# Kernel tuning notes

Hardware: AMD Instinct MI355X
Metric: run time of the kernel (lower is better)

Reference implementation:

```python
import jax, jax.numpy as jnp
import numpy as np

NEG_INF = -10000.0  # matches the original max_val init
EPS = 1e-8          # torch.nn.CosineSimilarity default eps


def setup_inputs() -> dict:
    key = jax.random.key(0)
    k1, k2, k3 = jax.random.split(key, 3)
    B, S, H = 32, 1024, 1024
    seq = jax.random.normal(k1, (B, S, H), dtype=jnp.float32)
    # sep0 = index of first [SEP] (end of question), sep1 = end of passage
    sep0 = jax.random.randint(k2, (B, 1), 32, 128)
    sep1 = jax.random.randint(k3, (B, 1), 768, S)
    idxs = jnp.concatenate([sep0, sep1], axis=1).astype(jnp.int64)
    return {"sequence_outputs": seq, "idxs": idxs, "max_ans_len": 32}


def reference(sequence_outputs, idxs, max_ans_len):
    # sequence_outputs: [B, S, H] float; idxs: [B, 2] int (sep0, sep1)
    B, S, H = sequence_outputs.shape
    L = max_ans_len
    sep0 = idxs[:, 0]
    sep1 = idxs[:, 1]

    # question_cat_repr = cat(seq[1], seq[sep0-1]); cos over the 2H concat
    # decomposes as (h_i.q1 + h_j.q2) / (sqrt(|h_i|^2+|h_j|^2) * |q|)
    q1 = sequence_outputs[:, 1, :]                                   # [B, H]
    q2 = jnp.take_along_axis(
        sequence_outputs, (sep0 - 1)[:, None, None], axis=1)[:, 0, :]  # [B, H]
    qn2 = jnp.sum(q1 * q1, -1) + jnp.sum(q2 * q2, -1)                # [B]

    d1 = jnp.einsum('bsh,bh->bs', sequence_outputs, q1)             # [B, S]
    d2 = jnp.einsum('bsh,bh->bs', sequence_outputs, q2)             # [B, S]
    n2 = jnp.sum(sequence_outputs * sequence_outputs, -1)           # [B, S]

    # banded window: for start i, ends j = i + l, l in [0, L)
    i = jnp.arange(S)[:, None]                                      # [S, 1]
    l = jnp.arange(L)[None, :]                                      # [1, L]
    j = jnp.minimum(i + l, S - 1)                                   # [S, L]
    d2w = d2[:, j]                                                  # [B, S, L]
    n2w = n2[:, j]                                                  # [B, S, L]

    denom = jnp.maximum(
        jnp.sqrt((n2[:, :, None] + n2w) * qn2[:, None, None]), EPS)
    sim = (d1[:, :, None] + d2w) / denom                            # [B, S, L]

    # valid ends: j = i + l < min(sep1, i + L); (i+l >= S implies invalid too)
    valid_j = (i + l)[None, :, :] < sep1[:, None, None]
    sim = jnp.where(valid_j, sim, NEG_INF)

    max_vals = jnp.max(sim, axis=-1)                                # [B, S]
    end_idx = jnp.arange(S)[None, :] + jnp.argmax(sim, axis=-1)     # [B, S]

    # valid starts: sep0 + 1 <= i < sep1
    pos = jnp.arange(S)[None, :]
    valid_i = (pos > sep0[:, None]) & (pos < sep1[:, None])
    max_vals = jnp.where(valid_i, max_vals, NEG_INF)
    end_idx = jnp.where(valid_i, end_idx, -1)
    return max_vals, end_idx
```

## Files before the change

kernel.cpp:

```cpp
#include <hip/hip_runtime.h>

#define NEG_INF_F (-10000.0f)
#define EPS_F (1e-8f)

typedef float f4 __attribute__((ext_vector_type(4)));

template <int H>
__global__ __launch_bounds__(256) void row_stats_pipe(
    const float* __restrict__ seq, const int* __restrict__ idxs,
    float* __restrict__ d1, float* __restrict__ d2, float* __restrict__ n2,
    int S, int nrows) {
  constexpr int NF4 = H / 4;
  constexpr int C = H / 256;
  constexpr int R = 4;
  int wave = blockIdx.x * 4 + (threadIdx.x >> 6);
  int lane = threadIdx.x & 63;
  int row0 = wave * R;
  if (row0 >= nrows) return;

  int b = row0 / S;
  int sep0 = idxs[2 * b];

  const f4* base = reinterpret_cast<const f4*>(seq);
  const f4* q1p = base + ((size_t)b * S + 1) * NF4 + lane;
  const f4* q2p = base + ((size_t)b * S + (sep0 - 1)) * NF4 + lane;
  const f4* rp = base + (size_t)row0 * NF4 + lane;

  f4 q1f[C], q2f[C], x[2][C];
  #pragma unroll
  for (int i = 0; i < C; ++i) q1f[i] = q1p[i * 64];
  #pragma unroll
  for (int i = 0; i < C; ++i) q2f[i] = q2p[i * 64];
  #pragma unroll
  for (int i = 0; i < C; ++i) x[0][i] = __builtin_nontemporal_load(rp + i * 64);

  #pragma unroll
  for (int r = 0; r < R; ++r) {
    if (r + 1 < R) {
      const f4* np = rp + (size_t)(r + 1) * NF4;
      #pragma unroll
      for (int i = 0; i < C; ++i)
        x[(r + 1) & 1][i] = __builtin_nontemporal_load(np + i * 64);
    }
    float s1 = 0.f, s2 = 0.f, sn = 0.f;
    #pragma unroll
    for (int i = 0; i < C; ++i) {
      f4 v = x[r & 1][i];
      s1 += v[0] * q1f[i][0] + v[1] * q1f[i][1] + v[2] * q1f[i][2] + v[3] * q1f[i][3];
      s2 += v[0] * q2f[i][0] + v[1] * q2f[i][1] + v[2] * q2f[i][2] + v[3] * q2f[i][3];
      sn += v[0] * v[0] + v[1] * v[1] + v[2] * v[2] + v[3] * v[3];
    }
    #pragma unroll
    for (int off = 32; off >= 1; off >>= 1) {
      s1 += __shfl_xor(s1, off, 64);
      s2 += __shfl_xor(s2, off, 64);
      sn += __shfl_xor(sn, off, 64);
    }
    if (lane == 0) {
      d1[row0 + r] = s1;
      d2[row0 + r] = s2;
      n2[row0 + r] = sn;
    }
  }
}

__global__ __launch_bounds__(256) void row_stats_kernel(
    const float* __restrict__ seq, const int* __restrict__ idxs,
    float* __restrict__ d1, float* __restrict__ d2, float* __restrict__ n2,
    int B, int S, int H) {
  int gtid = blockIdx.x * blockDim.x + threadIdx.x;
  int row = gtid >> 6;
  int lane = threadIdx.x & 63;
  int nrows = B * S;
  if (row >= nrows) return;

  int b = row / S;
  int sep0 = idxs[b * 2 + 0];

  const float* rowp = seq + (size_t)row * H;
  const float* q1p = seq + ((size_t)b * S + 1) * H;
  const float* q2p = seq + ((size_t)b * S + (sep0 - 1)) * H;

  float s1 = 0.f, s2 = 0.f, sn = 0.f;
  for (int h = lane * 4; h < H; h += 64 * 4) {
    float4 x = *reinterpret_cast<const float4*>(rowp + h);
    float4 a = *reinterpret_cast<const float4*>(q1p + h);
    float4 c = *reinterpret_cast<const float4*>(q2p + h);
    s1 += x.x * a.x + x.y * a.y + x.z * a.z + x.w * a.w;
    s2 += x.x * c.x + x.y * c.y + x.z * c.z + x.w * c.w;
    sn += x.x * x.x + x.y * x.y + x.z * x.z + x.w * x.w;
  }
  #pragma unroll
  for (int off = 32; off >= 1; off >>= 1) {
    s1 += __shfl_xor(s1, off, 64);
    s2 += __shfl_xor(s2, off, 64);
    sn += __shfl_xor(sn, off, 64);
  }
  if (lane == 0) {
    d1[row] = s1;
    d2[row] = s2;
    n2[row] = sn;
  }
}

template <int L>
__global__ __launch_bounds__(256) void window_max_wave(
    const float* __restrict__ d1, const float* __restrict__ d2,
    const float* __restrict__ n2, const int* __restrict__ idxs,
    float* __restrict__ out, int S, int nrows) {
  int wave = blockIdx.x * 4 + (threadIdx.x >> 6);
  int lane = threadIdx.x & 63;
  int h = lane >> 5;
  int l = lane & 31;
  int t = wave * 2 + h;
  if (t >= nrows) return;
  int b = t / S;
  int s = t - b * S;

  int sep0 = idxs[b * 2 + 0];
  int sep1 = idxs[b * 2 + 1];

  size_t bS = (size_t)b * S;
  float qn2 = n2[bS + 1] + n2[bS + (sep0 - 1)];
  float my_d1 = d1[t];
  float my_n2 = n2[t];

  int j = min(s + l, S - 1);
  float w2 = n2[bS + j];
  float v2 = d2[bS + j];
  float prod = (my_n2 + w2) * qn2;
  float sim = (my_d1 + v2) * __frsqrt_rn(fmaxf(prod, EPS_F * EPS_F));
  sim = (s + l < sep1) ? sim : NEG_INF_F;

  float best = sim;
  int best_l = l;
  #pragma unroll
  for (int off = 16; off >= 1; off >>= 1) {
    float ov = __shfl_xor(best, off, 64);
    int oi = __shfl_xor(best_l, off, 64);
    if (ov > best || (ov == best && oi < best_l)) {
      best = ov;
      best_l = oi;
    }
  }

  if (l == 0) {
    bool valid_i = (s > sep0) && (s < sep1);
    out[t] = valid_i ? best : NEG_INF_F;
    out[nrows + t] = valid_i ? (float)(s + best_l) : -1.0f;
  }
}

extern "C" void kernel_launch(void* const* d_in, const int* in_sizes, int n_in,
                              void* d_out, int out_size, void* d_ws, size_t ws_size,
                              hipStream_t stream) {
  const float* seq = (const float*)d_in[0];
  const int* idxs = (const int*)d_in[1];
  const int* pL = (const int*)d_in[2];

  int B = in_sizes[1] / 2;
  int S = out_size / (2 * B);
  int H = (int)((long long)in_sizes[0] / ((long long)B * S));
  int nrows = B * S;

  float* d1 = (float*)d_ws;
  float* d2 = d1 + nrows;
  float* n2 = d2 + nrows;

  if (H == 1024 && (S % 4) == 0 && (nrows % 16) == 0) {
    int gridA = nrows / 16;
    row_stats_pipe<1024><<<gridA, 256, 0, stream>>>(seq, idxs, d1, d2, n2, S,
                                                    nrows);
  } else {
    int gridA = (nrows + 3) / 4;
    row_stats_kernel<<<gridA, 256, 0, stream>>>(seq, idxs, d1, d2, n2, B, S, H);
  }

  int gridB = (nrows + 7) / 8;
  window_max_wave<32><<<gridB, 256, 0, stream>>>(d1, d2, n2, idxs,
                                                 (float*)d_out, S, nrows);
  (void)pL;
}
```

Measured before the change: 31.99 us.

## Stage query rows in LDS and compute window max one start per thread

```diff
diff --git a/kernel.cpp b/kernel.cpp
--- a/kernel.cpp
+++ b/kernel.cpp
@@ -6,31 +6,30 @@
 typedef float f4 __attribute__((ext_vector_type(4)));
 
 template <int H>
-__global__ __launch_bounds__(256) void row_stats_pipe(
+__global__ __launch_bounds__(256, 8) void row_stats_ldsq(
     const float* __restrict__ seq, const int* __restrict__ idxs,
     float* __restrict__ d1, float* __restrict__ d2, float* __restrict__ n2,
     int S, int nrows) {
   constexpr int NF4 = H / 4;
   constexpr int C = H / 256;
   constexpr int R = 4;
-  int wave = blockIdx.x * 4 + (threadIdx.x >> 6);
-  int lane = threadIdx.x & 63;
+  __shared__ f4 q1s[NF4];
+  __shared__ f4 q2s[NF4];
+
+  int tid = threadIdx.x;
+  int lane = tid & 63;
+  int wave = blockIdx.x * 4 + (tid >> 6);
   int row0 = wave * R;
-  if (row0 >= nrows) return;
-
-  int b = row0 / S;
+  int b = (blockIdx.x * 16) / S;
   int sep0 = idxs[2 * b];
 
   const f4* base = reinterpret_cast<const f4*>(seq);
-  const f4* q1p = base + ((size_t)b * S + 1) * NF4 + lane;
-  const f4* q2p = base + ((size_t)b * S + (sep0 - 1)) * NF4 + lane;
+  q1s[tid] = base[((size_t)b * S + 1) * NF4 + tid];
+  q2s[tid] = base[((size_t)b * S + (sep0 - 1)) * NF4 + tid];
+  __syncthreads();
+
   const f4* rp = base + (size_t)row0 * NF4 + lane;
-
-  f4 q1f[C], q2f[C], x[2][C];
-  #pragma unroll
-  for (int i = 0; i < C; ++i) q1f[i] = q1p[i * 64];
-  #pragma unroll
-  for (int i = 0; i < C; ++i) q2f[i] = q2p[i * 64];
+  f4 x[2][C];
   #pragma unroll
   for (int i = 0; i < C; ++i) x[0][i] = __builtin_nontemporal_load(rp + i * 64);
 
@@ -46,8 +45,10 @@
     #pragma unroll
     for (int i = 0; i < C; ++i) {
       f4 v = x[r & 1][i];
-      s1 += v[0] * q1f[i][0] + v[1] * q1f[i][1] + v[2] * q1f[i][2] + v[3] * q1f[i][3];
-      s2 += v[0] * q2f[i][0] + v[1] * q2f[i][1] + v[2] * q2f[i][2] + v[3] * q2f[i][3];
+      f4 a = q1s[i * 64 + lane];
+      f4 c = q2s[i * 64 + lane];
+      s1 += v[0] * a[0] + v[1] * a[1] + v[2] * a[2] + v[3] * a[3];
+      s2 += v[0] * c[0] + v[1] * c[1] + v[2] * c[2] + v[3] * c[3];
       sn += v[0] * v[0] + v[1] * v[1] + v[2] * v[2] + v[3] * v[3];
     }
     #pragma unroll
@@ -104,15 +105,11 @@
 }
 
 template <int L>
-__global__ __launch_bounds__(256) void window_max_wave(
+__global__ __launch_bounds__(64) void window_max_fast(
     const float* __restrict__ d1, const float* __restrict__ d2,
     const float* __restrict__ n2, const int* __restrict__ idxs,
     float* __restrict__ out, int S, int nrows) {
-  int wave = blockIdx.x * 4 + (threadIdx.x >> 6);
-  int lane = threadIdx.x & 63;
-  int h = lane >> 5;
-  int l = lane & 31;
-  int t = wave * 2 + h;
+  int t = blockIdx.x * 64 + threadIdx.x;
   if (t >= nrows) return;
   int b = t / S;
   int s = t - b * S;
@@ -125,30 +122,25 @@
   float my_d1 = d1[t];
   float my_n2 = n2[t];
 
-  int j = min(s + l, S - 1);
-  float w2 = n2[bS + j];
-  float v2 = d2[bS + j];
-  float prod = (my_n2 + w2) * qn2;
-  float sim = (my_d1 + v2) * __frsqrt_rn(fmaxf(prod, EPS_F * EPS_F));
-  sim = (s + l < sep1) ? sim : NEG_INF_F;
+  const float* d2b = d2 + bS;
+  const float* n2b = n2 + bS;
 
-  float best = sim;
-  int best_l = l;
+  float best = NEG_INF_F;
+  int best_l = 0;
   #pragma unroll
-  for (int off = 16; off >= 1; off >>= 1) {
-    float ov = __shfl_xor(best, off, 64);
-    int oi = __shfl_xor(best_l, off, 64);
-    if (ov > best || (ov == best && oi < best_l)) {
-      best = ov;
-      best_l = oi;
-    }
+  for (int l = 0; l < L; ++l) {
+    int j = min(s + l, S - 1);
+    float w2 = n2b[j];
+    float v2 = d2b[j];
+    float prod = (my_n2 + w2) * qn2;
+    float sim = (my_d1 + v2) * __frsqrt_rn(fmaxf(prod, EPS_F * EPS_F));
+    sim = (s + l < sep1) ? sim : NEG_INF_F;
+    if (sim > best) { best = sim; best_l = l; }
   }
 
-  if (l == 0) {
-    bool valid_i = (s > sep0) && (s < sep1);
-    out[t] = valid_i ? best : NEG_INF_F;
-    out[nrows + t] = valid_i ? (float)(s + best_l) : -1.0f;
-  }
+  bool valid_i = (s > sep0) && (s < sep1);
+  out[t] = valid_i ? best : NEG_INF_F;
+  out[nrows + t] = valid_i ? (float)(s + best_l) : -1.0f;
 }
 
 extern "C" void kernel_launch(void* const* d_in, const int* in_sizes, int n_in,
@@ -167,17 +159,17 @@
   float* d2 = d1 + nrows;
   float* n2 = d2 + nrows;
 
-  if (H == 1024 && (S % 4) == 0 && (nrows % 16) == 0) {
+  if (H == 1024 && (S % 16) == 0 && (nrows % 16) == 0) {
     int gridA = nrows / 16;
-    row_stats_pipe<1024><<<gridA, 256, 0, stream>>>(seq, idxs, d1, d2, n2, S,
+    row_stats_ldsq<1024><<<gridA, 256, 0, stream>>>(seq, idxs, d1, d2, n2, S,
                                                     nrows);
   } else {
     int gridA = (nrows + 3) / 4;
     row_stats_kernel<<<gridA, 256, 0, stream>>>(seq, idxs, d1, d2, n2, B, S, H);
   }
 
-  int gridB = (nrows + 7) / 8;
-  window_max_wave<32><<<gridB, 256, 0, stream>>>(d1, d2, n2, idxs,
-                                                 (float*)d_out, S, nrows);
+  int gridB = (nrows + 63) / 64;
+  window_max_fast<32><<<gridB, 64, 0, stream>>>(d1, d2, n2, idxs,
+                                                (float*)d_out, S, nrows);
   (void)pL;
 }
```

New measurement: 33.92 us. 1.06x slower.
